# Performance work log

Measured on AMD Instinct MI355X. Metric: run time of the kernel, lower is better.

Reference implementation:

```python
import jax, jax.numpy as jnp
import numpy as np

B, C, H, W = 16, 512, 64, 64
CB, CG = 64, 256  # bottleneck = C/8, g = C/2


def _conv1x1(x, w, b):
    # x: [B,Cin,H,W], w: [Cout,Cin] -> [B,Cout,H,W]
    return jnp.einsum('bchw,oc->bohw', x, w) + b[None, :, None, None]


def _avg_pool2(x):
    # 2x2 average pool, stride 2. x: [B,C,H,W] with even H,W.
    b, c, h, w = x.shape
    return x.reshape(b, c, h // 2, 2, w // 2, 2).mean(axis=(3, 5))


def setup_inputs() -> dict:
    key = jax.random.key(0)
    ks = jax.random.split(key, 6)
    s = 0.02
    return {
        'x': jax.random.normal(ks[0], (B, C, H, W), jnp.float32),
        'w_theta': jax.random.normal(ks[1], (CB, C), jnp.float32) * s,
        'b_theta': jnp.zeros((CB,), jnp.float32),
        'w_phi': jax.random.normal(ks[2], (CB, C), jnp.float32) * s,
        'b_phi': jnp.zeros((CB,), jnp.float32),
        'w_g': jax.random.normal(ks[3], (CG, C), jnp.float32) * s,
        'b_g': jnp.zeros((CG,), jnp.float32),
        'w_out': jax.random.normal(ks[4], (C, CG), jnp.float32) * s,
        'b_out': jnp.zeros((C,), jnp.float32),
        'gamma': jnp.zeros((1,), jnp.float32),
    }


def reference(x, w_theta, b_theta, w_phi, b_phi, w_g, b_g, w_out, b_out, gamma):
    b, c, h, w = x.shape
    n = h * w          # query locations
    m = n // 4         # pooled key/value locations

    theta = _conv1x1(x, w_theta, b_theta).reshape(b, CB, n)           # [B,CB,N]
    phi = _avg_pool2(_conv1x1(x, w_phi, b_phi)).reshape(b, CB, m)     # [B,CB,M]
    g = _avg_pool2(_conv1x1(x, w_g, b_g)).reshape(b, CG, m)           # [B,CG,M]

    logits = jnp.einsum('bcn,bcm->bnm', theta, phi)                   # [B,N,M]
    attn = jax.nn.softmax(logits, axis=-1)
    out = jnp.einsum('bcm,bnm->bcn', g, attn).reshape(b, CG, h, w)    # [B,CG,H,W]
    out = _conv1x1(out, w_out, b_out)                                 # [B,C,H,W]
    return gamma[0] * out + x
```

## Files before the change

kernel.cpp:

```cpp
#include <hip/hip_runtime.h>
#include <math.h>


typedef unsigned short u16;
typedef short bf16x8 __attribute__((ext_vector_type(8)));
typedef float f32x16 __attribute__((ext_vector_type(16)));
typedef u16 u16x4 __attribute__((ext_vector_type(4)));
typedef int i32x4 __attribute__((ext_vector_type(4)));

#define MFMA32 __builtin_amdgcn_mfma_f32_32x32x16_bf16
#define B_ 16
#define C_ 512
#define N_ 4096
#define M_ 1024
#define LOG2E 1.44269504088896f
#define FIXMAX 8.0f

__device__ __forceinline__ u16 f2b(float f) {
  unsigned u = __float_as_uint(f);
  return (u16)((u + 0x7FFFu + ((u >> 16) & 1u)) >> 16);
}
__device__ __forceinline__ unsigned cvtpk(float a, float b) {
  unsigned r;
  asm("v_cvt_pk_bf16_f32 %0, %1, %2" : "=v"(r) : "v"(a), "v"(b));
  return r;
}
__device__ __forceinline__ void permswap(unsigned &a, unsigned &b) {
  asm("v_permlane32_swap_b32 %0, %1" : "+v"(a), "+v"(b));
}
__device__ __forceinline__ float exp2v(float a) {
  float r;
  asm("v_exp_f32 %0, %1" : "=v"(r) : "v"(a));
  return r;
}
__device__ __forceinline__ void async_cp16(u16* lds, const u16* g) {
  __builtin_amdgcn_global_load_lds(
      (const __attribute__((address_space(1))) unsigned int*)g,
      (__attribute__((address_space(3))) unsigned int*)lds, 16, 0, 0);
}
__device__ __forceinline__ f32x16 fz16() {
  f32x16 z;
#pragma unroll
  for (int i = 0; i < 16; ++i) z[i] = 0.0f;
  return z;
}


__global__ __launch_bounds__(256) void cvt_all_kernel(
    const float* __restrict__ w_theta, const float* __restrict__ w_phi,
    const float* __restrict__ w_g, const float* __restrict__ w_out,
    const float* __restrict__ gamma, u16* __restrict__ dth, u16* __restrict__ dph,
    u16* __restrict__ dg, u16* __restrict__ dwo) {
  int i = blockIdx.x * 256 + threadIdx.x;
  if (i < 16384) {
    const float* s = (i < 8192) ? w_theta : w_phi;
    u16* d = (i < 8192) ? dth : dph;
    float scale = (i < 8192) ? LOG2E : 1.0f;
    int j = i & 8191;
    int o = j >> 7, c = (j & 127) * 4;
    float4 vv = *(const float4*)(s + (size_t)o * 512 + c);
    int idx = (((o >> 5) * 8 + (c >> 6)) * 4 + ((c >> 4) & 3)) * 512 +
              (((c >> 3) & 1) * 32 + (o & 31)) * 8 + (c & 7);
    u16x4 ot = {f2b(vv.x * scale), f2b(vv.y * scale), f2b(vv.z * scale), f2b(vv.w * scale)};
    *(u16x4*)(d + idx) = ot;
  } else if (i < 49152) {
    int j = i - 16384;
    int o = j >> 7, c = (j & 127) * 4;
    float4 vv = *(const float4*)(w_g + (size_t)o * 512 + c);
    int idx = (((o >> 5) * 8 + (c >> 6)) * 4 + ((c >> 4) & 3)) * 512 +
              (((c >> 3) & 1) * 32 + (o & 31)) * 8 + (c & 7);
    u16x4 ot = {f2b(vv.x), f2b(vv.y), f2b(vv.z), f2b(vv.w)};
    *(u16x4*)(dg + idx) = ot;
  } else {
    int j = i - 49152;
    int o = j >> 6, k = (j & 63) * 4;
    float scale = gamma[0];
    float4 vv = *(const float4*)(w_out + (size_t)o * 256 + k);
    int idx = ((o >> 5) * 16 + (k >> 4)) * 512 +
              (((k >> 3) & 1) * 32 + (o & 31)) * 8 + (k & 7);
    u16x4 ot = {f2b(vv.x * scale), f2b(vv.y * scale), f2b(vv.z * scale), f2b(vv.w * scale)};
    *(u16x4*)(dwo + idx) = ot;
  }
}

__global__ __launch_bounds__(512) void prep_kernel(
    const float* __restrict__ x, const u16* __restrict__ wth,
    const u16* __restrict__ wph, const u16* __restrict__ wg,
    const float* __restrict__ bth, const float* __restrict__ bph,
    const float* __restrict__ bg, u16* __restrict__ th, u16* __restrict__ ph,
    u16* __restrict__ vt) {
  __shared__ u16 xb[128 * 68];
  __shared__ u16 xpt[32 * 68];
  const int t = threadIdx.x;
  const int w = t >> 6, l = t & 63, lo = l & 31, hi = l >> 5;
  const int nb = blockIdx.x, b = blockIdx.y;
  const int n0 = nb * 128;
  const int lcol = (t & 31) * 4;
  const int lrow = t >> 5;

  f32x16 acc0 = fz16(), acc1 = fz16(), a_ph = fz16();

  float v[16];
  auto loadv = [&](int c0) {
#pragma unroll
    for (int i = 0; i < 4; ++i) {
      float4 f = *(const float4*)(x + ((size_t)(b * C_ + c0 + lrow + 16 * i)) * N_ + n0 + lcol);
      v[4*i] = f.x; v[4*i+1] = f.y; v[4*i+2] = f.z; v[4*i+3] = f.w;
    }
  };
  auto writeT = [&]() {
#pragma unroll
    for (int i = 0; i < 4; ++i) {
      int c = lrow + 16 * i;
      int blk = c >> 3;
#pragma unroll
      for (int k = 0; k < 4; ++k) {
        int n = lcol + k;
        int swz = ((n >> 2) ^ (n >> 5)) & 7;
        xb[n * 68 + ((blk ^ swz) * 8) + (c & 7)] = f2b(v[4*i+k]);
      }
    }
    float pA[4], pB[4];
#pragma unroll
    for (int i = 0; i < 4; ++i) {
      pA[i] = v[4*i] + v[4*i+1];
      pB[i] = v[4*i+2] + v[4*i+3];
    }
#pragma unroll
    for (int i = 0; i < 4; ++i) {
      pA[i] += __shfl_xor(pA[i], 16, 64);
      pB[i] += __shfl_xor(pB[i], 16, 64);
    }
    if ((t & 31) < 16) {
      int m0 = (t & 31) * 2;
#pragma unroll
      for (int i = 0; i < 4; ++i) {
        int c = lrow + 16 * i;
        xpt[m0 * 68 + c] = f2b(0.25f * pA[i]);
        xpt[(m0 + 1) * 68 + c] = f2b(0.25f * pB[i]);
      }
    }
  };
  auto domfma = [&](int c0b) {
    if (w < 4) {
      const int n = 32 * w + lo;
      const int rbase = n * 68;
      const int nswz = ((n >> 2) ^ (n >> 5)) & 7;
#pragma unroll
      for (int kh = 0; kh < 4; ++kh) {
        bf16x8 xa = *(const bf16x8*)(&xb[rbase + (((2*kh + hi) ^ nswz) * 8)]);
        bf16x8 w0 = *(const bf16x8*)(wth + ((c0b) * 4 + kh) * 512 + l * 8);
        bf16x8 w1 = *(const bf16x8*)(wth + ((8 + c0b) * 4 + kh) * 512 + l * 8);
        acc0 = MFMA32(xa, w0, acc0, 0, 0, 0);
        acc1 = MFMA32(xa, w1, acc1, 0, 0, 0);
      }
    } else {
      const int wg4 = w - 4;
      const u16* xpw = &xpt[lo * 68];
#pragma unroll
      for (int kh = 0; kh < 4; ++kh) {
        bf16x8 xp8 = *(const bf16x8*)(xpw + kh * 16 + hi * 8);
        bf16x8 g0 = *(const bf16x8*)(wg + ((16*wg4 + c0b) * 4 + kh) * 512 + l * 8);
        bf16x8 g1 = *(const bf16x8*)(wg + ((16*wg4 + 8 + c0b) * 4 + kh) * 512 + l * 8);
        acc0 = MFMA32(g0, xp8, acc0, 0, 0, 0);
        acc1 = MFMA32(g1, xp8, acc1, 0, 0, 0);
        if (wg4 < 2) {
          bf16x8 wp8 = *(const bf16x8*)(wph + ((wg4*8 + c0b) * 4 + kh) * 512 + l * 8);
          a_ph = MFMA32(xp8, wp8, a_ph, 0, 0, 0);
        }
      }
    }
  };

  loadv(0);
  for (int i = 0; i < 8; ++i) {
    if (i) __syncthreads();
    writeT();
    if (i < 7) loadv((i + 1) * 64);
    __syncthreads();
    domfma(i);
  }

  int rr[16];
#pragma unroll
  for (int r = 0; r < 16; ++r) rr[r] = (r & 3) + 8 * (r >> 2) + 4 * hi;

  if (w < 4) {
    u16* thb = th + (size_t)b * 262144;
#pragma unroll
    for (int r = 0; r < 16; ++r) {
      int sub = (((lo >> 3) & 1) * 32 + rr[r]) * 8 + (lo & 7);
      thb[((nb*4 + w)*4 + (lo >> 4)) * 512 + sub]     = f2b(acc0[r] + LOG2E * bth[lo]);
      thb[((nb*4 + w)*4 + 2 + (lo >> 4)) * 512 + sub] = f2b(acc1[r] + LOG2E * bth[32 + lo]);
    }
  } else {
    const int wg4 = w - 4;
    u16* vtb = vt + (size_t)b * 262144;
#pragma unroll
    for (int r = 0; r < 16; ++r) {
      int cg0 = 64 * wg4 + rr[r];
      int sub = (((lo >> 3) & 1) * 32 + rr[r]) * 8 + (lo & 7);
      int kk = (nb & 1) * 2 + (lo >> 4);
      vtb[(((nb >> 1) * 8 + 2*wg4) * 4 + kk) * 512 + sub]     = f2b(acc0[r] + bg[cg0]);
      vtb[(((nb >> 1) * 8 + 2*wg4 + 1) * 4 + kk) * 512 + sub] = f2b(acc1[r] + bg[cg0 + 32]);
    }
    if (wg4 < 2) {
      u16* phb = ph + (size_t)b * 65536;
#pragma unroll
      for (int r = 0; r < 16; ++r) {
        int sub = (((lo >> 3) & 1) * 32 + rr[r]) * 8 + (lo & 7);
        phb[(nb*4 + 2*wg4 + (lo >> 4)) * 512 + sub] = f2b(a_ph[r] + bph[32*wg4 + lo]);
      }
    }
  }
}

__global__ __launch_bounds__(512, 4) void attn_core_kernel(
    const u16* __restrict__ th, const u16* __restrict__ ph,
    const u16* __restrict__ vt, u16* __restrict__ Og) {
  __shared__ u16 smem[40960];

  const int t = threadIdx.x;
  const int w = t >> 6, l = t & 63;
  const int p = w & 3, h = w >> 2;
  const int flat = blockIdx.y * 32 + blockIdx.x;
  const int nf = (flat & 7) * 64 + (flat >> 3);
  const int b = nf >> 5, nb5 = nf & 31;
  const int jqt = nb5 * 4 + p;

  const u16* thb = th + (size_t)b * 262144;
  const u16* phb = ph + (size_t)b * 65536;
  const u16* vtb = vt + (size_t)b * 262144;

  bf16x8 thB[4];
#pragma unroll
  for (int kh = 0; kh < 4; ++kh)
    thB[kh] = *(const bf16x8*)(thb + (jqt * 4 + kh) * 512 + l * 8);

  f32x16 acc[4];
#pragma unroll
  for (int ct = 0; ct < 4; ++ct) acc[ct] = fz16();
  float sp[4] = {0.0f, 0.0f, 0.0f, 0.0f};

  auto stage = [&](int nbuf, int ic) {
    const int offu = w * 2560;
#pragma unroll
    for (int i = 0; i < 5; ++i) {
      int o = offu + i * 512;
      u16* dst = &smem[nbuf * 20480 + o];
      const u16* src = (o < 16384) ? (vtb + (size_t)ic * 16384 + o + l * 8)
                                   : (phb + (size_t)ic * 4096 + (o - 16384) + l * 8);
      async_cp16(dst, src);
    }
  };

  stage(0, 0);
  asm volatile("s_waitcnt vmcnt(0)" ::: "memory");
  __builtin_amdgcn_sched_barrier(0);
  __builtin_amdgcn_s_barrier();

  int buf = 0;
  for (int ic = 0; ic < 16; ++ic) {
    if (ic < 15) stage(buf ^ 1, ic + 1);

    const u16* Vs = &smem[buf * 20480];
    const u16* Ps = Vs + 16384;
#pragma unroll
    for (int jml = 0; jml < 2; ++jml) {
      bf16x8 pf[4];
#pragma unroll
      for (int kh = 0; kh < 4; ++kh)
        pf[kh] = *(const bf16x8*)(Ps + (jml * 4 + kh) * 512 + l * 8);
      f32x16 S = fz16();
#pragma unroll
      for (int kh = 0; kh < 4; ++kh) S = MFMA32(pf[kh], thB[kh], S, 0, 0, 0);

#pragma unroll
      for (int i = 0; i < 16; ++i) {
        S[i] = exp2v(S[i] - FIXMAX);
        sp[i & 3] += S[i];
      }

      bf16x8 Pf[2];
#pragma unroll
      for (int s = 0; s < 2; ++s) {
        unsigned a0 = cvtpk(S[8*s+0], S[8*s+1]);
        unsigned a1 = cvtpk(S[8*s+2], S[8*s+3]);
        unsigned a2 = cvtpk(S[8*s+4], S[8*s+5]);
        unsigned a3 = cvtpk(S[8*s+6], S[8*s+7]);
        permswap(a0, a2);
        permswap(a1, a3);
        i32x4 wv = {(int)a0, (int)a1, (int)a2, (int)a3};
        Pf[s] = __builtin_bit_cast(bf16x8, wv);
      }

      __builtin_amdgcn_s_setprio(1);
#pragma unroll
      for (int ct2 = 0; ct2 < 4; ++ct2) {
        const u16* vp = Vs + ((4 * h + ct2) * 4 + jml * 2) * 512 + l * 8;
        bf16x8 vf0 = *(const bf16x8*)(vp);
        bf16x8 vf1 = *(const bf16x8*)(vp + 512);
        acc[ct2] = MFMA32(vf0, Pf[0], acc[ct2], 0, 0, 0);
        acc[ct2] = MFMA32(vf1, Pf[1], acc[ct2], 0, 0, 0);
      }
      __builtin_amdgcn_s_setprio(0);
    }

    if (ic < 15) {
      asm volatile("s_waitcnt vmcnt(0)" ::: "memory");
      __builtin_amdgcn_sched_barrier(0);
      __builtin_amdgcn_s_barrier();
      buf ^= 1;
    }
  }

  float lsum = (sp[0] + sp[1]) + (sp[2] + sp[3]);
  lsum += __shfl_xor(lsum, 32, 64);
  const float linv = 1.0f / lsum;

  u16* Ob = Og + (size_t)b * 1048576 + (size_t)jqt * 16 * 512;
#pragma unroll
  for (int ct2 = 0; ct2 < 4; ++ct2) {
    f32x16& A = acc[ct2];
#pragma unroll
    for (int s = 0; s < 2; ++s) {
      unsigned a0 = cvtpk(A[8*s+0]*linv, A[8*s+1]*linv);
      unsigned a1 = cvtpk(A[8*s+2]*linv, A[8*s+3]*linv);
      unsigned a2 = cvtpk(A[8*s+4]*linv, A[8*s+5]*linv);
      unsigned a3 = cvtpk(A[8*s+6]*linv, A[8*s+7]*linv);
      permswap(a0, a2);
      permswap(a1, a3);
      i32x4 wv = {(int)a0, (int)a1, (int)a2, (int)a3};
      int f = 8 * h + 2 * ct2 + s;
      *(bf16x8*)(Ob + f * 512 + l * 8) = __builtin_bit_cast(bf16x8, wv);
    }
  }
}

__global__ __launch_bounds__(512, 4) void outconv_kernel(
    const u16* __restrict__ Og, const u16* __restrict__ wo,
    const float* __restrict__ b_out, const float* __restrict__ gamma,
    const float* __restrict__ x, float* __restrict__ out) {
  const int t = threadIdx.x;
  const int w = t >> 6, l = t & 63, lo = l & 31, hi = l >> 5;
  const int p = w & 3, h = w >> 2;
  const int flat = blockIdx.y * 32 + blockIdx.x;
  const int nf = (flat & 7) * 64 + (flat >> 3);
  const int b = nf >> 5, nb5 = nf & 31;
  const int jqt = nb5 * 4 + p;
  const int qp = jqt * 32;

  const u16* Ob = Og + (size_t)b * 1048576 + (size_t)jqt * 16 * 512;
  bf16x8 Of[16];
#pragma unroll
  for (int f = 0; f < 16; ++f)
    Of[f] = *(const bf16x8*)(Ob + f * 512 + l * 8);

  int rr[16];
#pragma unroll
  for (int r = 0; r < 16; ++r) rr[r] = (r & 3) + 8 * (r >> 2) + 4 * hi;

  const float gamma0 = gamma[0];
  for (int ctc = 0; ctc < 8; ++ctc) {
    f32x16 facc = fz16();
    const u16* wp = wo + (size_t)((8 * h + ctc) * 16) * 512 + l * 8;
#pragma unroll
    for (int f = 0; f < 16; ++f) {
      bf16x8 wfr = *(const bf16x8*)(wp + f * 512);
      facc = MFMA32(wfr, Of[f], facc, 0, 0, 0);
    }
#pragma unroll
    for (int r = 0; r < 16; ++r) {
      int c = 256 * h + 32 * ctc + rr[r];
      size_t idx = ((size_t)(b * C_ + c)) * N_ + qp + lo;
      float xv = __builtin_nontemporal_load(&x[idx]);
      __builtin_nontemporal_store(facc[r] + gamma0 * b_out[c] + xv, &out[idx]);
    }
  }
}

extern "C" void kernel_launch(void* const* d_in, const int* in_sizes, int n_in,
                              void* d_out, int out_size, void* d_ws, size_t ws_size,
                              hipStream_t stream) {
  (void)in_sizes; (void)n_in; (void)out_size; (void)ws_size;
  const float* x       = (const float*)d_in[0];
  const float* w_theta = (const float*)d_in[1];
  const float* b_theta = (const float*)d_in[2];
  const float* w_phi   = (const float*)d_in[3];
  const float* b_phi   = (const float*)d_in[4];
  const float* w_g     = (const float*)d_in[5];
  const float* b_g     = (const float*)d_in[6];
  const float* w_out   = (const float*)d_in[7];
  const float* b_out   = (const float*)d_in[8];
  const float* gamma   = (const float*)d_in[9];
  float* out = (float*)d_out;

  char* ws = (char*)d_ws;
  u16* th  = (u16*)(ws);
  u16* ph  = (u16*)(ws + 8388608);
  u16* vt  = (u16*)(ws + 10485760);
  u16* wth = (u16*)(ws + 18874368);
  u16* wph = (u16*)(ws + 18939904);
  u16* wg  = (u16*)(ws + 19005440);
  u16* wo  = (u16*)(ws + 19267584);
  u16* Og  = (u16*)(ws + 19529728);

  cvt_all_kernel<<<320, 256, 0, stream>>>(w_theta, w_phi, w_g, w_out, gamma,
                                          wth, wph, wg, wo);
  prep_kernel<<<dim3(32, 16), 512, 0, stream>>>(x, wth, wph, wg, b_theta, b_phi,
                                                b_g, th, ph, vt);
  attn_core_kernel<<<dim3(32, 16), 512, 0, stream>>>(th, ph, vt, Og);
  outconv_kernel<<<dim3(32, 16), 512, 0, stream>>>(Og, wo, b_out, gamma, x, out);
}
```

Baseline: 172.4 us.

## Split attention K/V staging into half-chunks with 4-buffer, depth-2 async prefetch

Each 64-key chunk stage is split into two 32-key half-stages, each holding 16 KB of V and 4 KB of phi, rotated through four LDS buffers. Two stages are kept in flight and the loop waits with vmcnt(3), so only the older stage must land before compute. This gives finer-grained overlap between global-to-LDS loads and the MFMA/exp work and hides more load latency. The cost is twice as many barriers per chunk and a more complex counter discipline. LDS usage stays at 40960 halves.

```diff
diff --git a/kernel.cpp b/kernel.cpp
--- a/kernel.cpp
+++ b/kernel.cpp
@@ -242,75 +242,80 @@
   for (int ct = 0; ct < 4; ++ct) acc[ct] = fz16();
   float sp[4] = {0.0f, 0.0f, 0.0f, 0.0f};
 
-  auto stage = [&](int nbuf, int ic) {
-    const int offu = w * 2560;
-#pragma unroll
-    for (int i = 0; i < 5; ++i) {
-      int o = offu + i * 512;
-      u16* dst = &smem[nbuf * 20480 + o];
-      const u16* src = (o < 16384) ? (vtb + (size_t)ic * 16384 + o + l * 8)
-                                   : (phb + (size_t)ic * 4096 + (o - 16384) + l * 8);
-      async_cp16(dst, src);
+  auto stage = [&](int k) {
+    const int ic = k >> 1, jml = k & 1;
+    u16* base = &smem[(k & 3) * 10240];
+#pragma unroll
+    for (int i = 0; i < 2; ++i) {
+      int o = t * 8 + i * 4096;
+      const u16* src = vtb + (size_t)(ic * 32 + (o >> 10) * 4 + 2 * jml) * 512 + (o & 1023);
+      async_cp16(base + o, src);
+    }
+    {
+      int o = (t & 255) * 8;
+      const u16* src = phb + (size_t)((2 * ic + jml) * 4) * 512 + o;
+      async_cp16(base + 8192 + o, src);
     }
   };
 
-  stage(0, 0);
-  asm volatile("s_waitcnt vmcnt(0)" ::: "memory");
+  stage(0);
+  stage(1);
+  asm volatile("s_waitcnt vmcnt(3)" ::: "memory");
   __builtin_amdgcn_sched_barrier(0);
   __builtin_amdgcn_s_barrier();
 
-  int buf = 0;
-  for (int ic = 0; ic < 16; ++ic) {
-    if (ic < 15) stage(buf ^ 1, ic + 1);
-
-    const u16* Vs = &smem[buf * 20480];
-    const u16* Ps = Vs + 16384;
-#pragma unroll
-    for (int jml = 0; jml < 2; ++jml) {
-      bf16x8 pf[4];
-#pragma unroll
-      for (int kh = 0; kh < 4; ++kh)
-        pf[kh] = *(const bf16x8*)(Ps + (jml * 4 + kh) * 512 + l * 8);
-      f32x16 S = fz16();
-#pragma unroll
-      for (int kh = 0; kh < 4; ++kh) S = MFMA32(pf[kh], thB[kh], S, 0, 0, 0);
-
-#pragma unroll
-      for (int i = 0; i < 16; ++i) {
-        S[i] = exp2v(S[i] - FIXMAX);
-        sp[i & 3] += S[i];
-      }
-
-      bf16x8 Pf[2];
-#pragma unroll
-      for (int s = 0; s < 2; ++s) {
-        unsigned a0 = cvtpk(S[8*s+0], S[8*s+1]);
-        unsigned a1 = cvtpk(S[8*s+2], S[8*s+3]);
-        unsigned a2 = cvtpk(S[8*s+4], S[8*s+5]);
-        unsigned a3 = cvtpk(S[8*s+6], S[8*s+7]);
-        permswap(a0, a2);
-        permswap(a1, a3);
-        i32x4 wv = {(int)a0, (int)a1, (int)a2, (int)a3};
-        Pf[s] = __builtin_bit_cast(bf16x8, wv);
-      }
-
-      __builtin_amdgcn_s_setprio(1);
-#pragma unroll
-      for (int ct2 = 0; ct2 < 4; ++ct2) {
-        const u16* vp = Vs + ((4 * h + ct2) * 4 + jml * 2) * 512 + l * 8;
-        bf16x8 vf0 = *(const bf16x8*)(vp);
-        bf16x8 vf1 = *(const bf16x8*)(vp + 512);
-        acc[ct2] = MFMA32(vf0, Pf[0], acc[ct2], 0, 0, 0);
-        acc[ct2] = MFMA32(vf1, Pf[1], acc[ct2], 0, 0, 0);
-      }
-      __builtin_amdgcn_s_setprio(0);
-    }
-
-    if (ic < 15) {
+#pragma unroll 4
+  for (int k = 0; k < 32; ++k) {
+    if (k < 30) stage(k + 2);
+
+    const u16* Vs = &smem[(k & 3) * 10240];
+    const u16* Ps = Vs + 8192;
+
+    f32x16 S = fz16();
+#pragma unroll
+    for (int kh = 0; kh < 4; ++kh) {
+      bf16x8 pf = *(const bf16x8*)(Ps + kh * 512 + l * 8);
+      S = MFMA32(pf, thB[kh], S, 0, 0, 0);
+    }
+
+#pragma unroll
+    for (int i = 0; i < 16; ++i) {
+      S[i] = exp2v(S[i] - FIXMAX);
+      sp[i & 3] += S[i];
+    }
+
+    bf16x8 Pf[2];
+#pragma unroll
+    for (int s = 0; s < 2; ++s) {
+      unsigned a0 = cvtpk(S[8*s+0], S[8*s+1]);
+      unsigned a1 = cvtpk(S[8*s+2], S[8*s+3]);
+      unsigned a2 = cvtpk(S[8*s+4], S[8*s+5]);
+      unsigned a3 = cvtpk(S[8*s+6], S[8*s+7]);
+      permswap(a0, a2);
+      permswap(a1, a3);
+      i32x4 wv = {(int)a0, (int)a1, (int)a2, (int)a3};
+      Pf[s] = __builtin_bit_cast(bf16x8, wv);
+    }
+
+    __builtin_amdgcn_s_setprio(1);
+#pragma unroll
+    for (int ct2 = 0; ct2 < 4; ++ct2) {
+      const u16* vp = Vs + (size_t)((4 * h + ct2) * 2) * 512 + l * 8;
+      bf16x8 vf0 = *(const bf16x8*)(vp);
+      bf16x8 vf1 = *(const bf16x8*)(vp + 512);
+      acc[ct2] = MFMA32(vf0, Pf[0], acc[ct2], 0, 0, 0);
+      acc[ct2] = MFMA32(vf1, Pf[1], acc[ct2], 0, 0, 0);
+    }
+    __builtin_amdgcn_s_setprio(0);
+
+    if (k < 30) {
+      asm volatile("s_waitcnt vmcnt(3)" ::: "memory");
+      __builtin_amdgcn_sched_barrier(0);
+      __builtin_amdgcn_s_barrier();
+    } else if (k == 30) {
       asm volatile("s_waitcnt vmcnt(0)" ::: "memory");
       __builtin_amdgcn_sched_barrier(0);
       __builtin_amdgcn_s_barrier();
-      buf ^= 1;
     }
   }
 
```

After: 243.7 us. +41.4%, slower.
